# Kernel tuning notes

Measured on AMD Instinct MI355X. Metric: run time of the kernel, lower is better.

## Reference

```python
import jax, jax.numpy as jnp
import numpy as np

P = 16          # patch size
D = 256         # emb dim
NH = 4          # attention heads
DH = D // NH    # head dim
GS = 4          # LE-fusion group size
EPS = 1e-5
ALPHA = 1.0
DELTA = 1.0
BETA = 1.0


def setup_inputs() -> dict:
    key = jax.random.key(0)
    ks = jax.random.split(key, 12)
    B, C, H, W = 8, 1, 256, 256
    s = 0.02
    return {
        "x": jax.random.normal(ks[0], (B, C, H, W), jnp.float32),
        # patch embed as matmul over flattened patches (equivalent to Conv2d k=s=P)
        "Wp": jax.random.normal(ks[1], (C * P * P, D), jnp.float32) * s,
        "bp": jnp.zeros((D,), jnp.float32),
        "ln_g": jnp.ones((D,), jnp.float32),
        "ln_b": jnp.zeros((D,), jnp.float32),
        "Wq": jax.random.normal(ks[2], (D, D), jnp.float32) * s,
        "bq": jnp.zeros((D,), jnp.float32),
        "Wk": jax.random.normal(ks[3], (D, D), jnp.float32) * s,
        "bk": jnp.zeros((D,), jnp.float32),
        "Wv": jax.random.normal(ks[4], (D, D), jnp.float32) * s,
        "bv": jnp.zeros((D,), jnp.float32),
        "Wo": jax.random.normal(ks[5], (D, D), jnp.float32) * s,
        "bo": jnp.zeros((D,), jnp.float32),
    }


def _forward(x, Wp, bp, ln_g, ln_b, Wq, bq, Wk, bk, Wv, bv, Wo, bo):
    B, C, H, W = x.shape
    nh, nw = H // P, W // P
    N = nh * nw
    # --- patch embed: (B,C,H,W) -> (B,N,C*P*P) @ Wp ---
    patches = x.reshape(B, C, nh, P, nw, P).transpose(0, 2, 4, 1, 3, 5)
    patches = patches.reshape(B, N, C * P * P)
    z = patches @ Wp + bp  # (B, N, D)
    # --- NF-Norm: LayerNorm then NeuroFocal scaling ---
    mu = z.mean(-1, keepdims=True)
    var = ((z - mu) ** 2).mean(-1, keepdims=True)
    zn = (z - mu) * jax.lax.rsqrt(var + EPS) * ln_g + ln_b
    mu2 = zn.mean(-1, keepdims=True)
    var2 = ((zn - mu2) ** 2).mean(-1, keepdims=True)
    nf = jnp.abs(zn - mu2).sum(-1, keepdims=True) / (jnp.sqrt(var2 + EPS) + EPS)
    z = zn * (1.0 + nf)
    # --- AG-NFA attention ---
    def split(t):  # (B,N,D) -> (B,NH,N,DH)
        return t.reshape(B, N, NH, DH).transpose(0, 2, 1, 3)
    Q = split(z @ Wq + bq)
    K = split(z @ Wk + bk)
    V = split(z @ Wv + bv)
    qk = jnp.einsum("bhnd,bhmd->bhnm", Q, K)
    logits = qk / jnp.sqrt(jnp.float32(DH))
    mu_q = Q.mean(-1, keepdims=True)
    var_q = ((Q - mu_q) ** 2).mean(-1, keepdims=True)
    sigma_q = jnp.sqrt(var_q + EPS)
    nf_q = jnp.abs(Q - mu_q).sum(-1, keepdims=True) / (sigma_q + EPS)  # (B,NH,N,1)
    # ||Q_n - K_m||^2 = |Q|^2 + |K|^2 - 2 Q.K  (avoids O(N^2*d) diff tensor)
    q2 = (Q * Q).sum(-1)  # (B,NH,N)
    k2 = (K * K).sum(-1)  # (B,NH,N)
    omega = q2[..., :, None] + k2[..., None, :] - 2.0 * qk
    omega = omega / (jnp.exp(-DELTA * nf_q) + 1.0)
    A = jax.nn.softmax(logits - ALPHA * omega, axis=-1)
    out = jnp.einsum("bhnm,bhmd->bhnd", A, V)
    out = out.transpose(0, 2, 1, 3).reshape(B, N, D)
    Y = out @ Wo + bo
    # --- LE-Fusion ---
    G = N // GS
    Yg = Y.reshape(B, G, GS, D)
    E = jnp.linalg.norm(Yg, axis=-1)  # (B,G,GS)
    lam = jax.nn.softmax(BETA * E, axis=-1)[..., None]
    return (lam * Yg).sum(axis=2)  # (B, G, D)


def reference(x, Wp, bp, ln_g, ln_b, Wq, bq, Wk, bk, Wv, bv, Wo, bo):
    return _forward(x, Wp, bp, ln_g, ln_b, Wq, bq, Wk, bk, Wv, bv, Wo, bo)
```

## Files before the change

### kernel.cpp

```cpp
#include <hip/hip_runtime.h>

#define EPSF 1e-5f
#define KSTR 68
#define PSTR 260

#define FMA4(ACC, ZS, WV) \
    ACC.x = fmaf(ZS, WV.x, ACC.x); ACC.y = fmaf(ZS, WV.y, ACC.y); \
    ACC.z = fmaf(ZS, WV.z, ACC.z); ACC.w = fmaf(ZS, WV.w, ACC.w);

__global__ __launch_bounds__(512, 2) void ka_patch_nf_qkv(
    const float* __restrict__ x,
    const float* __restrict__ Wp, const float* __restrict__ bp,
    const float* __restrict__ ln_g, const float* __restrict__ ln_b,
    const float* __restrict__ Wq, const float* __restrict__ bq,
    const float* __restrict__ Wk, const float* __restrict__ bk,
    const float* __restrict__ Wv, const float* __restrict__ bv,
    float* __restrict__ Qg, float* __restrict__ Kg, float* __restrict__ Vg)
{
    extern __shared__ float sm[];
    float* zr = sm;
    float* ps = sm + 2048;

    const int tid = threadIdx.x;
    const int kq = tid >> 7, tg = (tid >> 6) & 1, ln = tid & 63;
    const int wave = tid >> 6, lane = tid & 63;
    const int tok0 = blockIdx.x * 8;
    const int tg4 = 4 * tg;

    #pragma unroll
    for (int i = 0; i < 4; ++i) {
        int e = tid + 512 * i;
        int t = e >> 8, dd = e & 255;
        int tk = tok0 + t, b = tk >> 8, n = tk & 255;
        int ph = n >> 4, pw = n & 15, p = dd >> 4, q = dd & 15;
        zr[t * 256 + dd] = x[b * 65536 + (ph * 16 + p) * 256 + pw * 16 + q];
    }
    __syncthreads();

    {
        const float* wr = Wp + kq * 16384 + 4 * ln;
        const float* zb = zr + tg4 * 256 + kq * 64;
        float4 a0 = make_float4(0.f,0.f,0.f,0.f), a1 = a0, a2 = a0, a3 = a0;
        #pragma unroll
        for (int kk = 0; kk < 64; kk += 8) {
            float4 w0 = *(const float4*)(wr + (kk + 0) * 256);
            float4 w1 = *(const float4*)(wr + (kk + 1) * 256);
            float4 w2 = *(const float4*)(wr + (kk + 2) * 256);
            float4 w3 = *(const float4*)(wr + (kk + 3) * 256);
            float4 w4 = *(const float4*)(wr + (kk + 4) * 256);
            float4 w5 = *(const float4*)(wr + (kk + 5) * 256);
            float4 w6 = *(const float4*)(wr + (kk + 6) * 256);
            float4 w7 = *(const float4*)(wr + (kk + 7) * 256);
            float4 zA0 = *(const float4*)(zb + 0 * 256 + kk);
            float4 zA1 = *(const float4*)(zb + 0 * 256 + kk + 4);
            float4 zB0 = *(const float4*)(zb + 1 * 256 + kk);
            float4 zB1 = *(const float4*)(zb + 1 * 256 + kk + 4);
            float4 zC0 = *(const float4*)(zb + 2 * 256 + kk);
            float4 zC1 = *(const float4*)(zb + 2 * 256 + kk + 4);
            float4 zD0 = *(const float4*)(zb + 3 * 256 + kk);
            float4 zD1 = *(const float4*)(zb + 3 * 256 + kk + 4);
            FMA4(a0, zA0.x, w0) FMA4(a0, zA0.y, w1) FMA4(a0, zA0.z, w2) FMA4(a0, zA0.w, w3)
            FMA4(a0, zA1.x, w4) FMA4(a0, zA1.y, w5) FMA4(a0, zA1.z, w6) FMA4(a0, zA1.w, w7)
            FMA4(a1, zB0.x, w0) FMA4(a1, zB0.y, w1) FMA4(a1, zB0.z, w2) FMA4(a1, zB0.w, w3)
            FMA4(a1, zB1.x, w4) FMA4(a1, zB1.y, w5) FMA4(a1, zB1.z, w6) FMA4(a1, zB1.w, w7)
            FMA4(a2, zC0.x, w0) FMA4(a2, zC0.y, w1) FMA4(a2, zC0.z, w2) FMA4(a2, zC0.w, w3)
            FMA4(a2, zC1.x, w4) FMA4(a2, zC1.y, w5) FMA4(a2, zC1.z, w6) FMA4(a2, zC1.w, w7)
            FMA4(a3, zD0.x, w0) FMA4(a3, zD0.y, w1) FMA4(a3, zD0.z, w2) FMA4(a3, zD0.w, w3)
            FMA4(a3, zD1.x, w4) FMA4(a3, zD1.y, w5) FMA4(a3, zD1.z, w6) FMA4(a3, zD1.w, w7)
        }
        float* pp = ps + kq * 2048 + tg4 * 256 + 4 * ln;
        *(float4*)(pp + 0 * 256) = a0;
        *(float4*)(pp + 1 * 256) = a1;
        *(float4*)(pp + 2 * 256) = a2;
        *(float4*)(pp + 3 * 256) = a3;
    }
    __syncthreads();
    {
        int e = tid * 4;
        float4 u0 = *(float4*)(ps + e);
        float4 u1 = *(float4*)(ps + 2048 + e);
        float4 u2 = *(float4*)(ps + 4096 + e);
        float4 u3 = *(float4*)(ps + 6144 + e);
        float4 bb = *(const float4*)(bp + (e & 255));
        float4 z;
        z.x = (u0.x + u1.x) + (u2.x + u3.x) + bb.x;
        z.y = (u0.y + u1.y) + (u2.y + u3.y) + bb.y;
        z.z = (u0.z + u1.z) + (u2.z + u3.z) + bb.z;
        z.w = (u0.w + u1.w) + (u2.w + u3.w) + bb.w;
        *(float4*)(zr + e) = z;
    }
    __syncthreads();

    {
        float g[4], bb2[4], v[4];
        #pragma unroll
        for (int c = 0; c < 4; ++c) { g[c] = ln_g[lane + 64 * c]; bb2[c] = ln_b[lane + 64 * c]; }
        float s = 0.f, ss = 0.f;
        #pragma unroll
        for (int c = 0; c < 4; ++c) { v[c] = zr[wave * 256 + lane + 64 * c]; s += v[c]; ss += v[c] * v[c]; }
        #pragma unroll
        for (int o = 32; o; o >>= 1) { s += __shfl_xor(s, o); ss += __shfl_xor(ss, o); }
        float mu  = s * (1.f / 256.f);
        float var = ss * (1.f / 256.f) - mu * mu;
        float rs  = rsqrtf(var + EPSF);
        float zn[4]; float s2 = 0.f, ss2 = 0.f;
        #pragma unroll
        for (int c = 0; c < 4; ++c) {
            zn[c] = (v[c] - mu) * rs * g[c] + bb2[c];
            s2 += zn[c]; ss2 += zn[c] * zn[c];
        }
        #pragma unroll
        for (int o = 32; o; o >>= 1) { s2 += __shfl_xor(s2, o); ss2 += __shfl_xor(ss2, o); }
        float mu2  = s2 * (1.f / 256.f);
        float var2 = ss2 * (1.f / 256.f) - mu2 * mu2;
        float as = 0.f;
        #pragma unroll
        for (int c = 0; c < 4; ++c) as += fabsf(zn[c] - mu2);
        #pragma unroll
        for (int o = 32; o; o >>= 1) as += __shfl_xor(as, o);
        float nf = as / (sqrtf(var2 + EPSF) + EPSF);
        float sc = 1.f + nf;
        #pragma unroll
        for (int c = 0; c < 4; ++c) zr[wave * 256 + lane + 64 * c] = zn[c] * sc;
    }
    __syncthreads();

    {
        const float* qr = Wq + kq * 16384 + 4 * ln;
        const float* kr = Wk + kq * 16384 + 4 * ln;
        const float* vr = Wv + kq * 16384 + 4 * ln;
        const float* zb = zr + tg4 * 256 + kq * 64;
        float4 aq0 = make_float4(0.f,0.f,0.f,0.f), aq1 = aq0, aq2 = aq0, aq3 = aq0;
        float4 ak0 = aq0, ak1 = aq0, ak2 = aq0, ak3 = aq0;
        float4 av0 = aq0, av1 = aq0, av2 = aq0, av3 = aq0;
        #pragma unroll
        for (int kk = 0; kk < 64; kk += 4) {
            float4 qw0 = *(const float4*)(qr + (kk + 0) * 256);
            float4 qw1 = *(const float4*)(qr + (kk + 1) * 256);
            float4 qw2 = *(const float4*)(qr + (kk + 2) * 256);
            float4 qw3 = *(const float4*)(qr + (kk + 3) * 256);
            float4 kw0 = *(const float4*)(kr + (kk + 0) * 256);
            float4 kw1 = *(const float4*)(kr + (kk + 1) * 256);
            float4 kw2 = *(const float4*)(kr + (kk + 2) * 256);
            float4 kw3 = *(const float4*)(kr + (kk + 3) * 256);
            float4 vw0 = *(const float4*)(vr + (kk + 0) * 256);
            float4 vw1 = *(const float4*)(vr + (kk + 1) * 256);
            float4 vw2 = *(const float4*)(vr + (kk + 2) * 256);
            float4 vw3 = *(const float4*)(vr + (kk + 3) * 256);
            float4 zA = *(const float4*)(zb + 0 * 256 + kk);
            float4 zB = *(const float4*)(zb + 1 * 256 + kk);
            float4 zC = *(const float4*)(zb + 2 * 256 + kk);
            float4 zD = *(const float4*)(zb + 3 * 256 + kk);
            FMA4(aq0, zA.x, qw0) FMA4(aq0, zA.y, qw1) FMA4(aq0, zA.z, qw2) FMA4(aq0, zA.w, qw3)
            FMA4(ak0, zA.x, kw0) FMA4(ak0, zA.y, kw1) FMA4(ak0, zA.z, kw2) FMA4(ak0, zA.w, kw3)
            FMA4(av0, zA.x, vw0) FMA4(av0, zA.y, vw1) FMA4(av0, zA.z, vw2) FMA4(av0, zA.w, vw3)
            FMA4(aq1, zB.x, qw0) FMA4(aq1, zB.y, qw1) FMA4(aq1, zB.z, qw2) FMA4(aq1, zB.w, qw3)
            FMA4(ak1, zB.x, kw0) FMA4(ak1, zB.y, kw1) FMA4(ak1, zB.z, kw2) FMA4(ak1, zB.w, kw3)
            FMA4(av1, zB.x, vw0) FMA4(av1, zB.y, vw1) FMA4(av1, zB.z, vw2) FMA4(av1, zB.w, vw3)
            FMA4(aq2, zC.x, qw0) FMA4(aq2, zC.y, qw1) FMA4(aq2, zC.z, qw2) FMA4(aq2, zC.w, qw3)
            FMA4(ak2, zC.x, kw0) FMA4(ak2, zC.y, kw1) FMA4(ak2, zC.z, kw2) FMA4(ak2, zC.w, kw3)
            FMA4(av2, zC.x, vw0) FMA4(av2, zC.y, vw1) FMA4(av2, zC.z, vw2) FMA4(av2, zC.w, vw3)
            FMA4(aq3, zD.x, qw0) FMA4(aq3, zD.y, qw1) FMA4(aq3, zD.z, qw2) FMA4(aq3, zD.w, qw3)
            FMA4(ak3, zD.x, kw0) FMA4(ak3, zD.y, kw1) FMA4(ak3, zD.z, kw2) FMA4(ak3, zD.w, kw3)
            FMA4(av3, zD.x, vw0) FMA4(av3, zD.y, vw1) FMA4(av3, zD.z, vw2) FMA4(av3, zD.w, vw3)
        }
        float* pq = ps + kq * 2048 + tg4 * 256 + 4 * ln;
        *(float4*)(pq + 0 * 256) = aq0;
        *(float4*)(pq + 1 * 256) = aq1;
        *(float4*)(pq + 2 * 256) = aq2;
        *(float4*)(pq + 3 * 256) = aq3;
        float* pk = pq + 8192;
        *(float4*)(pk + 0 * 256) = ak0;
        *(float4*)(pk + 1 * 256) = ak1;
        *(float4*)(pk + 2 * 256) = ak2;
        *(float4*)(pk + 3 * 256) = ak3;
        float* pv = pq + 16384;
        *(float4*)(pv + 0 * 256) = av0;
        *(float4*)(pv + 1 * 256) = av1;
        *(float4*)(pv + 2 * 256) = av2;
        *(float4*)(pv + 3 * 256) = av3;
    }
    __syncthreads();

    {
        int e = tid * 4, t = e >> 8, d0 = e & 255;
        int tk = tok0 + t, b = tk >> 8, n = tk & 255;
        int h = d0 >> 6, dh = d0 & 63;
        #pragma unroll
        for (int mat = 0; mat < 3; ++mat) {
            const float* pr = ps + mat * 8192;
            float4 u0 = *(float4*)(pr + e);
            float4 u1 = *(float4*)(pr + 2048 + e);
            float4 u2 = *(float4*)(pr + 4096 + e);
            float4 u3 = *(float4*)(pr + 6144 + e);
            const float* bsrc = (mat == 0) ? bq : (mat == 1) ? bk : bv;
            float4 bb = *(const float4*)(bsrc + d0);
            float4 o;
            o.x = (u0.x + u1.x) + (u2.x + u3.x) + bb.x;
            o.y = (u0.y + u1.y) + (u2.y + u3.y) + bb.y;
            o.z = (u0.z + u1.z) + (u2.z + u3.z) + bb.z;
            o.w = (u0.w + u1.w) + (u2.w + u3.w) + bb.w;
            float* gout = ((mat == 0) ? Qg : (mat == 1) ? Kg : Vg)
                        + ((b * 4 + h) * 256 + n) * 64 + dh;
            *(float4*)gout = o;
        }
    }
}

__global__ __launch_bounds__(512, 2) void kb_attn(
    const float* __restrict__ Qg, const float* __restrict__ Kg,
    const float* __restrict__ Vg, float* __restrict__ Og)
{
    extern __shared__ float lds[];
    float* Kl = lds;
    float* k2 = lds + 256 * KSTR;
    float* Pl = lds;

    const int tid = threadIdx.x;
    const int xcd = blockIdx.x & 7, slot = blockIdx.x >> 3;
    const int bh = xcd * 4 + (slot >> 3);
    const int qt = slot & 7;

    const float* Qb = Qg + (bh * 256 + qt * 32) * 64;
    const float* Kb = Kg + bh * 16384;
    const float* Vb = Vg + bh * 16384;

    const int q = tid >> 4;
    const int r = tid & 15;

    {
        const float4* Ks = (const float4*)Kb;
        #pragma unroll
        for (int i = 0; i < 8; ++i) {
            int flat = tid + 512 * i;
            int row = flat >> 4, c4 = flat & 15;
            *(float4*)(Kl + row * KSTR + c4 * 4) = Ks[flat];
        }
    }
    __syncthreads();

    {
        int row = tid >> 1, half = tid & 1;
        const float* kp = Kl + row * KSTR + half * 32;
        float ssq = 0.f;
        #pragma unroll
        for (int c = 0; c < 8; ++c) {
            float4 kv = *(const float4*)(kp + 4 * c);
            ssq += kv.x*kv.x + kv.y*kv.y + kv.z*kv.z + kv.w*kv.w;
        }
        ssq += __shfl_xor(ssq, 1);
        if (half == 0) k2[row] = ssq;
    }

    float4 Qr[16];
    {
        const float4* Qp = (const float4*)(Qb + q * 64);
        #pragma unroll
        for (int c = 0; c < 16; ++c) Qr[c] = Qp[c];
    }
    float fq, gq, iq;
    {
        float s = 0.f, ss = 0.f;
        #pragma unroll
        for (int c = 0; c < 16; ++c) {
            float4 v = Qr[c];
            s  += v.x + v.y + v.z + v.w;
            ss += v.x*v.x + v.y*v.y + v.z*v.z + v.w*v.w;
        }
        float mu = s * (1.f / 64.f);
        float as = 0.f;
        #pragma unroll
        for (int c = 0; c < 16; ++c) {
            float4 v = Qr[c];
            as += fabsf(v.x - mu) + fabsf(v.y - mu)
                + fabsf(v.z - mu) + fabsf(v.w - mu);
        }
        float var = ss * (1.f / 64.f) - mu * mu;
        float sg  = sqrtf(var + EPSF);
        float nf  = as / (sg + EPSF);
        float inv = 1.f / (__expf(-nf) + 1.f);
        fq = 0.125f + 2.f * inv;
        gq = ss * inv;
        iq = inv;
    }
    __syncthreads();

    float s_[16];
    #pragma unroll
    for (int j = 0; j < 16; ++j) {
        int m = r + 16 * j;
        const float* kp = Kl + m * KSTR;
        float acc = 0.f;
        #pragma unroll
        for (int c = 0; c < 16; ++c) {
            float4 kv = *(const float4*)(kp + 4 * c);
            acc += Qr[c].x*kv.x + Qr[c].y*kv.y + Qr[c].z*kv.z + Qr[c].w*kv.w;
        }
        s_[j] = acc * fq - gq - k2[m] * iq;
    }

    float M = s_[0];
    #pragma unroll
    for (int j = 1; j < 16; ++j) M = fmaxf(M, s_[j]);
    #pragma unroll
    for (int o = 1; o < 16; o <<= 1) M = fmaxf(M, __shfl_xor(M, o));
    float L = 0.f;
    #pragma unroll
    for (int j = 0; j < 16; ++j) { s_[j] = __expf(s_[j] - M); L += s_[j]; }
    #pragma unroll
    for (int o = 1; o < 16; o <<= 1) L += __shfl_xor(L, o);
    float invL = 1.f / L;

    __syncthreads();
    #pragma unroll
    for (int j = 0; j < 16; ++j) Pl[q * PSTR + r + 16 * j] = s_[j] * invL;
    __syncthreads();

    float4 a0 = make_float4(0.f, 0.f, 0.f, 0.f);
    const float* pq = Pl + q * PSTR;
    #pragma unroll 8
    for (int m = 0; m < 256; ++m) {
        float pw = pq[m];
        float4 v = *(const float4*)(Vb + m * 64 + 4 * r);
        a0.x = fmaf(pw, v.x, a0.x); a0.y = fmaf(pw, v.y, a0.y);
        a0.z = fmaf(pw, v.z, a0.z); a0.w = fmaf(pw, v.w, a0.w);
    }
    {
        int b = bh >> 2, h = bh & 3;
        int n = qt * 32 + q;
        float* op = Og + (b * 256 + n) * 256 + h * 64 + 4 * r;
        *(float4*)op = a0;
    }
}

__global__ __launch_bounds__(512, 2) void kc_wo_le(
    const float* __restrict__ Og, const float* __restrict__ Wo,
    const float* __restrict__ bo, float* __restrict__ out)
{
    __shared__ __align__(16) float sm[2048 + 8192 + 8];
    float* yr  = sm;
    float* ps  = sm + 2048;
    float* red = sm + 10240;

    const int tid = threadIdx.x;
    const int kq = tid >> 7, tg = (tid >> 6) & 1, ln = tid & 63;
    const int wave = tid >> 6, lane = tid & 63;
    const int tok0 = blockIdx.x * 8;
    const int tg4 = 4 * tg;

    *(float4*)(yr + tid * 4) = *(const float4*)(Og + tok0 * 256 + tid * 4);
    __syncthreads();

    {
        const float* wr = Wo + kq * 16384 + 4 * ln;
        const float* zb = yr + tg4 * 256 + kq * 64;
        float4 a0 = make_float4(0.f,0.f,0.f,0.f), a1 = a0, a2 = a0, a3 = a0;
        #pragma unroll
        for (int kk = 0; kk < 64; kk += 8) {
            float4 w0 = *(const float4*)(wr + (kk + 0) * 256);
            float4 w1 = *(const float4*)(wr + (kk + 1) * 256);
            float4 w2 = *(const float4*)(wr + (kk + 2) * 256);
            float4 w3 = *(const float4*)(wr + (kk + 3) * 256);
            float4 w4 = *(const float4*)(wr + (kk + 4) * 256);
            float4 w5 = *(const float4*)(wr + (kk + 5) * 256);
            float4 w6 = *(const float4*)(wr + (kk + 6) * 256);
            float4 w7 = *(const float4*)(wr + (kk + 7) * 256);
            float4 zA0 = *(const float4*)(zb + 0 * 256 + kk);
            float4 zA1 = *(const float4*)(zb + 0 * 256 + kk + 4);
            float4 zB0 = *(const float4*)(zb + 1 * 256 + kk);
            float4 zB1 = *(const float4*)(zb + 1 * 256 + kk + 4);
            float4 zC0 = *(const float4*)(zb + 2 * 256 + kk);
            float4 zC1 = *(const float4*)(zb + 2 * 256 + kk + 4);
            float4 zD0 = *(const float4*)(zb + 3 * 256 + kk);
            float4 zD1 = *(const float4*)(zb + 3 * 256 + kk + 4);
            FMA4(a0, zA0.x, w0) FMA4(a0, zA0.y, w1) FMA4(a0, zA0.z, w2) FMA4(a0, zA0.w, w3)
            FMA4(a0, zA1.x, w4) FMA4(a0, zA1.y, w5) FMA4(a0, zA1.z, w6) FMA4(a0, zA1.w, w7)
            FMA4(a1, zB0.x, w0) FMA4(a1, zB0.y, w1) FMA4(a1, zB0.z, w2) FMA4(a1, zB0.w, w3)
            FMA4(a1, zB1.x, w4) FMA4(a1, zB1.y, w5) FMA4(a1, zB1.z, w6) FMA4(a1, zB1.w, w7)
            FMA4(a2, zC0.x, w0) FMA4(a2, zC0.y, w1) FMA4(a2, zC0.z, w2) FMA4(a2, zC0.w, w3)
            FMA4(a2, zC1.x, w4) FMA4(a2, zC1.y, w5) FMA4(a2, zC1.z, w6) FMA4(a2, zC1.w, w7)
            FMA4(a3, zD0.x, w0) FMA4(a3, zD0.y, w1) FMA4(a3, zD0.z, w2) FMA4(a3, zD0.w, w3)
            FMA4(a3, zD1.x, w4) FMA4(a3, zD1.y, w5) FMA4(a3, zD1.z, w6) FMA4(a3, zD1.w, w7)
        }
        float* pp = ps + kq * 2048 + tg4 * 256 + 4 * ln;
        *(float4*)(pp + 0 * 256) = a0;
        *(float4*)(pp + 1 * 256) = a1;
        *(float4*)(pp + 2 * 256) = a2;
        *(float4*)(pp + 3 * 256) = a3;
    }
    __syncthreads();
    {
        int e = tid * 4;
        float4 u0 = *(float4*)(ps + e);
        float4 u1 = *(float4*)(ps + 2048 + e);
        float4 u2 = *(float4*)(ps + 4096 + e);
        float4 u3 = *(float4*)(ps + 6144 + e);
        float4 bb = *(const float4*)(bo + (e & 255));
        float4 y;
        y.x = (u0.x + u1.x) + (u2.x + u3.x) + bb.x;
        y.y = (u0.y + u1.y) + (u2.y + u3.y) + bb.y;
        y.z = (u0.z + u1.z) + (u2.z + u3.z) + bb.z;
        y.w = (u0.w + u1.w) + (u2.w + u3.w) + bb.w;
        *(float4*)(yr + e) = y;
    }
    __syncthreads();
    {
        float ssq = 0.f;
        #pragma unroll
        for (int c = 0; c < 4; ++c) {
            float v = yr[wave * 256 + lane + 64 * c];
            ssq += v * v;
        }
        #pragma unroll
        for (int o = 32; o; o >>= 1) ssq += __shfl_xor(ssq, o);
        if (lane == 0) red[wave] = sqrtf(ssq);
    }
    __syncthreads();
    {
        int g = tid >> 8, d = tid & 255;
        float e0 = red[4 * g], e1 = red[4 * g + 1], e2 = red[4 * g + 2], e3 = red[4 * g + 3];
        float m = fmaxf(fmaxf(e0, e1), fmaxf(e2, e3));
        float x0 = __expf(e0 - m), x1 = __expf(e1 - m), x2 = __expf(e2 - m), x3 = __expf(e3 - m);
        float inv = 1.f / (x0 + x1 + x2 + x3);
        float val = (x0 * yr[(4 * g) * 256 + d] + x1 * yr[(4 * g + 1) * 256 + d]
                   + x2 * yr[(4 * g + 2) * 256 + d] + x3 * yr[(4 * g + 3) * 256 + d]) * inv;
        out[(blockIdx.x * 2 + g) * 256 + d] = val;
    }
}

extern "C" void kernel_launch(void* const* d_in, const int* in_sizes, int n_in,
                              void* d_out, int out_size, void* d_ws, size_t ws_size,
                              hipStream_t stream) {
    const float* x    = (const float*)d_in[0];
    const float* Wp   = (const float*)d_in[1];
    const float* bp   = (const float*)d_in[2];
    const float* ln_g = (const float*)d_in[3];
    const float* ln_b = (const float*)d_in[4];
    const float* Wq   = (const float*)d_in[5];
    const float* bq   = (const float*)d_in[6];
    const float* Wk   = (const float*)d_in[7];
    const float* bk   = (const float*)d_in[8];
    const float* Wv   = (const float*)d_in[9];
    const float* bv   = (const float*)d_in[10];
    const float* Wo   = (const float*)d_in[11];
    const float* bo   = (const float*)d_in[12];
    float* out = (float*)d_out;

    float* ws = (float*)d_ws;
    const size_t TKD = 2048 * 64 * 4;
    float* Qg = ws;
    float* Kg = ws + TKD;
    float* Vg = ws + 2 * TKD;
    float* Og = ws + 3 * TKD;

    const int ka_lds = (2048 + 3 * 4 * 2048) * 4;
    const int kb_lds = (256 * KSTR + 256) * 4;
    (void)hipFuncSetAttribute((const void*)ka_patch_nf_qkv,
                              hipFuncAttributeMaxDynamicSharedMemorySize, ka_lds);
    (void)hipFuncSetAttribute((const void*)kb_attn,
                              hipFuncAttributeMaxDynamicSharedMemorySize, kb_lds);

    ka_patch_nf_qkv<<<256, 512, ka_lds, stream>>>(x, Wp, bp, ln_g, ln_b,
                                                  Wq, bq, Wk, bk, Wv, bv, Qg, Kg, Vg);
    kb_attn<<<256, 512, kb_lds, stream>>>(Qg, Kg, Vg, Og);
    kc_wo_le<<<256, 512, 0, stream>>>(Og, Wo, bo, out);
}
```

Baseline: 60.70 us.

## Double block size and split GEMM K-dimension eight ways in projection kernels

The patch-embed/QKV kernel and the Wo/LE-fusion kernel now launch 1024 threads and split each GEMM's reduction dimension across eight thread groups instead of four. Partial sums are combined through LDS by the first 512 threads. The fused QKV pass is replaced by three sequential single-matrix passes, which shrinks LDS and register use. The aim is more parallelism and latency hiding per block, paid for with extra barriers, more partial-sum traffic and some idle threads during the combine and norm phases.

```diff
diff --git a/kernel.cpp b/kernel.cpp
--- a/kernel.cpp
+++ b/kernel.cpp
@@ -8,7 +8,59 @@
     ACC.x = fmaf(ZS, WV.x, ACC.x); ACC.y = fmaf(ZS, WV.y, ACC.y); \
     ACC.z = fmaf(ZS, WV.z, ACC.z); ACC.w = fmaf(ZS, WV.w, ACC.w);
 
-__global__ __launch_bounds__(512, 2) void ka_patch_nf_qkv(
+__device__ __forceinline__ void gemm_pass8(
+    const float* __restrict__ W, const float* __restrict__ zr,
+    float* __restrict__ ps, int kq, int tg4, int ln)
+{
+    const float* wr = W + kq * 8192 + 4 * ln;
+    const float* zb = zr + tg4 * 256 + kq * 32;
+    float4 a0 = make_float4(0.f,0.f,0.f,0.f), a1 = a0, a2 = a0, a3 = a0;
+    #pragma unroll
+    for (int kk = 0; kk < 32; kk += 8) {
+        float4 w0 = *(const float4*)(wr + (kk + 0) * 256);
+        float4 w1 = *(const float4*)(wr + (kk + 1) * 256);
+        float4 w2 = *(const float4*)(wr + (kk + 2) * 256);
+        float4 w3 = *(const float4*)(wr + (kk + 3) * 256);
+        float4 w4 = *(const float4*)(wr + (kk + 4) * 256);
+        float4 w5 = *(const float4*)(wr + (kk + 5) * 256);
+        float4 w6 = *(const float4*)(wr + (kk + 6) * 256);
+        float4 w7 = *(const float4*)(wr + (kk + 7) * 256);
+        float4 zA0 = *(const float4*)(zb + 0 * 256 + kk);
+        float4 zA1 = *(const float4*)(zb + 0 * 256 + kk + 4);
+        float4 zB0 = *(const float4*)(zb + 1 * 256 + kk);
+        float4 zB1 = *(const float4*)(zb + 1 * 256 + kk + 4);
+        float4 zC0 = *(const float4*)(zb + 2 * 256 + kk);
+        float4 zC1 = *(const float4*)(zb + 2 * 256 + kk + 4);
+        float4 zD0 = *(const float4*)(zb + 3 * 256 + kk);
+        float4 zD1 = *(const float4*)(zb + 3 * 256 + kk + 4);
+        FMA4(a0, zA0.x, w0) FMA4(a0, zA0.y, w1) FMA4(a0, zA0.z, w2) FMA4(a0, zA0.w, w3)
+        FMA4(a0, zA1.x, w4) FMA4(a0, zA1.y, w5) FMA4(a0, zA1.z, w6) FMA4(a0, zA1.w, w7)
+        FMA4(a1, zB0.x, w0) FMA4(a1, zB0.y, w1) FMA4(a1, zB0.z, w2) FMA4(a1, zB0.w, w3)
+        FMA4(a1, zB1.x, w4) FMA4(a1, zB1.y, w5) FMA4(a1, zB1.z, w6) FMA4(a1, zB1.w, w7)
+        FMA4(a2, zC0.x, w0) FMA4(a2, zC0.y, w1) FMA4(a2, zC0.z, w2) FMA4(a2, zC0.w, w3)
+        FMA4(a2, zC1.x, w4) FMA4(a2, zC1.y, w5) FMA4(a2, zC1.z, w6) FMA4(a2, zC1.w, w7)
+        FMA4(a3, zD0.x, w0) FMA4(a3, zD0.y, w1) FMA4(a3, zD0.z, w2) FMA4(a3, zD0.w, w3)
+        FMA4(a3, zD1.x, w4) FMA4(a3, zD1.y, w5) FMA4(a3, zD1.z, w6) FMA4(a3, zD1.w, w7)
+    }
+    float* pp = ps + kq * 2048 + tg4 * 256 + 4 * ln;
+    *(float4*)(pp + 0 * 256) = a0;
+    *(float4*)(pp + 1 * 256) = a1;
+    *(float4*)(pp + 2 * 256) = a2;
+    *(float4*)(pp + 3 * 256) = a3;
+}
+
+__device__ __forceinline__ float4 combine8(const float* __restrict__ ps, int e)
+{
+    float4 a = *(const float4*)(ps + e);
+    #pragma unroll
+    for (int kq = 1; kq < 8; ++kq) {
+        float4 u = *(const float4*)(ps + kq * 2048 + e);
+        a.x += u.x; a.y += u.y; a.z += u.z; a.w += u.w;
+    }
+    return a;
+}
+
+__global__ __launch_bounds__(1024, 4) void ka_patch_nf_qkv(
     const float* __restrict__ x,
     const float* __restrict__ Wp, const float* __restrict__ bp,
     const float* __restrict__ ln_g, const float* __restrict__ ln_b,
@@ -27,71 +79,28 @@
     const int tok0 = blockIdx.x * 8;
     const int tg4 = 4 * tg;
 
-    #pragma unroll
-    for (int i = 0; i < 4; ++i) {
-        int e = tid + 512 * i;
+    {
+        int e = tid * 2;
         int t = e >> 8, dd = e & 255;
         int tk = tok0 + t, b = tk >> 8, n = tk & 255;
         int ph = n >> 4, pw = n & 15, p = dd >> 4, q = dd & 15;
-        zr[t * 256 + dd] = x[b * 65536 + (ph * 16 + p) * 256 + pw * 16 + q];
-    }
-    __syncthreads();
-
-    {
-        const float* wr = Wp + kq * 16384 + 4 * ln;
-        const float* zb = zr + tg4 * 256 + kq * 64;
-        float4 a0 = make_float4(0.f,0.f,0.f,0.f), a1 = a0, a2 = a0, a3 = a0;
-        #pragma unroll
-        for (int kk = 0; kk < 64; kk += 8) {
-            float4 w0 = *(const float4*)(wr + (kk + 0) * 256);
-            float4 w1 = *(const float4*)(wr + (kk + 1) * 256);
-            float4 w2 = *(const float4*)(wr + (kk + 2) * 256);
-            float4 w3 = *(const float4*)(wr + (kk + 3) * 256);
-            float4 w4 = *(const float4*)(wr + (kk + 4) * 256);
-            float4 w5 = *(const float4*)(wr + (kk + 5) * 256);
-            float4 w6 = *(const float4*)(wr + (kk + 6) * 256);
-            float4 w7 = *(const float4*)(wr + (kk + 7) * 256);
-            float4 zA0 = *(const float4*)(zb + 0 * 256 + kk);
-            float4 zA1 = *(const float4*)(zb + 0 * 256 + kk + 4);
-            float4 zB0 = *(const float4*)(zb + 1 * 256 + kk);
-            float4 zB1 = *(const float4*)(zb + 1 * 256 + kk + 4);
-            float4 zC0 = *(const float4*)(zb + 2 * 256 + kk);
-            float4 zC1 = *(const float4*)(zb + 2 * 256 + kk + 4);
-            float4 zD0 = *(const float4*)(zb + 3 * 256 + kk);
-            float4 zD1 = *(const float4*)(zb + 3 * 256 + kk + 4);
-            FMA4(a0, zA0.x, w0) FMA4(a0, zA0.y, w1) FMA4(a0, zA0.z, w2) FMA4(a0, zA0.w, w3)
-            FMA4(a0, zA1.x, w4) FMA4(a0, zA1.y, w5) FMA4(a0, zA1.z, w6) FMA4(a0, zA1.w, w7)
-            FMA4(a1, zB0.x, w0) FMA4(a1, zB0.y, w1) FMA4(a1, zB0.z, w2) FMA4(a1, zB0.w, w3)
-            FMA4(a1, zB1.x, w4) FMA4(a1, zB1.y, w5) FMA4(a1, zB1.z, w6) FMA4(a1, zB1.w, w7)
-            FMA4(a2, zC0.x, w0) FMA4(a2, zC0.y, w1) FMA4(a2, zC0.z, w2) FMA4(a2, zC0.w, w3)
-            FMA4(a2, zC1.x, w4) FMA4(a2, zC1.y, w5) FMA4(a2, zC1.z, w6) FMA4(a2, zC1.w, w7)
-            FMA4(a3, zD0.x, w0) FMA4(a3, zD0.y, w1) FMA4(a3, zD0.z, w2) FMA4(a3, zD0.w, w3)
-            FMA4(a3, zD1.x, w4) FMA4(a3, zD1.y, w5) FMA4(a3, zD1.z, w6) FMA4(a3, zD1.w, w7)
-        }
-        float* pp = ps + kq * 2048 + tg4 * 256 + 4 * ln;
-        *(float4*)(pp + 0 * 256) = a0;
-        *(float4*)(pp + 1 * 256) = a1;
-        *(float4*)(pp + 2 * 256) = a2;
-        *(float4*)(pp + 3 * 256) = a3;
-    }
-    __syncthreads();
-    {
+        float2 v = *(const float2*)(x + b * 65536 + (ph * 16 + p) * 256 + pw * 16 + q);
+        *(float2*)(zr + e) = v;
+    }
+    __syncthreads();
+
+    gemm_pass8(Wp, zr, ps, kq, tg4, ln);
+    __syncthreads();
+    if (tid < 512) {
         int e = tid * 4;
-        float4 u0 = *(float4*)(ps + e);
-        float4 u1 = *(float4*)(ps + 2048 + e);
-        float4 u2 = *(float4*)(ps + 4096 + e);
-        float4 u3 = *(float4*)(ps + 6144 + e);
+        float4 a = combine8(ps, e);
         float4 bb = *(const float4*)(bp + (e & 255));
-        float4 z;
-        z.x = (u0.x + u1.x) + (u2.x + u3.x) + bb.x;
-        z.y = (u0.y + u1.y) + (u2.y + u3.y) + bb.y;
-        z.z = (u0.z + u1.z) + (u2.z + u3.z) + bb.z;
-        z.w = (u0.w + u1.w) + (u2.w + u3.w) + bb.w;
-        *(float4*)(zr + e) = z;
-    }
-    __syncthreads();
-
-    {
+        a.x += bb.x; a.y += bb.y; a.z += bb.z; a.w += bb.w;
+        *(float4*)(zr + e) = a;
+    }
+    __syncthreads();
+
+    if (wave < 8) {
         float g[4], bb2[4], v[4];
         #pragma unroll
         for (int c = 0; c < 4; ++c) { g[c] = ln_g[lane + 64 * c]; bb2[c] = ln_b[lane + 64 * c]; }
@@ -126,83 +135,38 @@
     __syncthreads();
 
     {
-        const float* qr = Wq + kq * 16384 + 4 * ln;
-        const float* kr = Wk + kq * 16384 + 4 * ln;
-        const float* vr = Wv + kq * 16384 + 4 * ln;
-        const float* zb = zr + tg4 * 256 + kq * 64;
-        float4 aq0 = make_float4(0.f,0.f,0.f,0.f), aq1 = aq0, aq2 = aq0, aq3 = aq0;
-        float4 ak0 = aq0, ak1 = aq0, ak2 = aq0, ak3 = aq0;
-        float4 av0 = aq0, av1 = aq0, av2 = aq0, av3 = aq0;
-        #pragma unroll
-        for (int kk = 0; kk < 64; kk += 4) {
-            float4 qw0 = *(const float4*)(qr + (kk + 0) * 256);
-            float4 qw1 = *(const float4*)(qr + (kk + 1) * 256);
-            float4 qw2 = *(const float4*)(qr + (kk + 2) * 256);
-            float4 qw3 = *(const float4*)(qr + (kk + 3) * 256);
-            float4 kw0 = *(const float4*)(kr + (kk + 0) * 256);
-            float4 kw1 = *(const float4*)(kr + (kk + 1) * 256);
-            float4 kw2 = *(const float4*)(kr + (kk + 2) * 256);
-            float4 kw3 = *(const float4*)(kr + (kk + 3) * 256);
-            float4 vw0 = *(const float4*)(vr + (kk + 0) * 256);
-            float4 vw1 = *(const float4*)(vr + (kk + 1) * 256);
-            float4 vw2 = *(const float4*)(vr + (kk + 2) * 256);
-            float4 vw3 = *(const float4*)(vr + (kk + 3) * 256);
-            float4 zA = *(const float4*)(zb + 0 * 256 + kk);
-            float4 zB = *(const float4*)(zb + 1 * 256 + kk);
-            float4 zC = *(const float4*)(zb + 2 * 256 + kk);
-            float4 zD = *(const float4*)(zb + 3 * 256 + kk);
-            FMA4(aq0, zA.x, qw0) FMA4(aq0, zA.y, qw1) FMA4(aq0, zA.z, qw2) FMA4(aq0, zA.w, qw3)
-            FMA4(ak0, zA.x, kw0) FMA4(ak0, zA.y, kw1) FMA4(ak0, zA.z, kw2) FMA4(ak0, zA.w, kw3)
-            FMA4(av0, zA.x, vw0) FMA4(av0, zA.y, vw1) FMA4(av0, zA.z, vw2) FMA4(av0, zA.w, vw3)
-            FMA4(aq1, zB.x, qw0) FMA4(aq1, zB.y, qw1) FMA4(aq1, zB.z, qw2) FMA4(aq1, zB.w, qw3)
-            FMA4(ak1, zB.x, kw0) FMA4(ak1, zB.y, kw1) FMA4(ak1, zB.z, kw2) FMA4(ak1, zB.w, kw3)
-            FMA4(av1, zB.x, vw0) FMA4(av1, zB.y, vw1) FMA4(av1, zB.z, vw2) FMA4(av1, zB.w, vw3)
-            FMA4(aq2, zC.x, qw0) FMA4(aq2, zC.y, qw1) FMA4(aq2, zC.z, qw2) FMA4(aq2, zC.w, qw3)
-            FMA4(ak2, zC.x, kw0) FMA4(ak2, zC.y, kw1) FMA4(ak2, zC.z, kw2) FMA4(ak2, zC.w, kw3)
-            FMA4(av2, zC.x, vw0) FMA4(av2, zC.y, vw1) FMA4(av2, zC.z, vw2) FMA4(av2, zC.w, vw3)
-            FMA4(aq3, zD.x, qw0) FMA4(aq3, zD.y, qw1) FMA4(aq3, zD.z, qw2) FMA4(aq3, zD.w, qw3)
-            FMA4(ak3, zD.x, kw0) FMA4(ak3, zD.y, kw1) FMA4(ak3, zD.z, kw2) FMA4(ak3, zD.w, kw3)
-            FMA4(av3, zD.x, vw0) FMA4(av3, zD.y, vw1) FMA4(av3, zD.z, vw2) FMA4(av3, zD.w, vw3)
-        }
-        float* pq = ps + kq * 2048 + tg4 * 256 + 4 * ln;
-        *(float4*)(pq + 0 * 256) = aq0;
-        *(float4*)(pq + 1 * 256) = aq1;
-        *(float4*)(pq + 2 * 256) = aq2;
-        *(float4*)(pq + 3 * 256) = aq3;
-        float* pk = pq + 8192;
-        *(float4*)(pk + 0 * 256) = ak0;
-        *(float4*)(pk + 1 * 256) = ak1;
-        *(float4*)(pk + 2 * 256) = ak2;
-        *(float4*)(pk + 3 * 256) = ak3;
-        float* pv = pq + 16384;
-        *(float4*)(pv + 0 * 256) = av0;
-        *(float4*)(pv + 1 * 256) = av1;
-        *(float4*)(pv + 2 * 256) = av2;
-        *(float4*)(pv + 3 * 256) = av3;
-    }
-    __syncthreads();
-
-    {
         int e = tid * 4, t = e >> 8, d0 = e & 255;
         int tk = tok0 + t, b = tk >> 8, n = tk & 255;
         int h = d0 >> 6, dh = d0 & 63;
-        #pragma unroll
-        for (int mat = 0; mat < 3; ++mat) {
-            const float* pr = ps + mat * 8192;
-            float4 u0 = *(float4*)(pr + e);
-            float4 u1 = *(float4*)(pr + 2048 + e);
-            float4 u2 = *(float4*)(pr + 4096 + e);
-            float4 u3 = *(float4*)(pr + 6144 + e);
-            const float* bsrc = (mat == 0) ? bq : (mat == 1) ? bk : bv;
-            float4 bb = *(const float4*)(bsrc + d0);
-            float4 o;
-            o.x = (u0.x + u1.x) + (u2.x + u3.x) + bb.x;
-            o.y = (u0.y + u1.y) + (u2.y + u3.y) + bb.y;
-            o.z = (u0.z + u1.z) + (u2.z + u3.z) + bb.z;
-            o.w = (u0.w + u1.w) + (u2.w + u3.w) + bb.w;
-            float* gout = ((mat == 0) ? Qg : (mat == 1) ? Kg : Vg)
-                        + ((b * 4 + h) * 256 + n) * 64 + dh;
-            *(float4*)gout = o;
+        const long goff = ((long)(b * 4 + h) * 256 + n) * 64 + dh;
+
+        gemm_pass8(Wq, zr, ps, kq, tg4, ln);
+        __syncthreads();
+        if (tid < 512) {
+            float4 a = combine8(ps, e);
+            float4 bb = *(const float4*)(bq + d0);
+            a.x += bb.x; a.y += bb.y; a.z += bb.z; a.w += bb.w;
+            *(float4*)(Qg + goff) = a;
+        }
+        __syncthreads();
+
+        gemm_pass8(Wk, zr, ps, kq, tg4, ln);
+        __syncthreads();
+        if (tid < 512) {
+            float4 a = combine8(ps, e);
+            float4 bb = *(const float4*)(bk + d0);
+            a.x += bb.x; a.y += bb.y; a.z += bb.z; a.w += bb.w;
+            *(float4*)(Kg + goff) = a;
+        }
+        __syncthreads();
+
+        gemm_pass8(Wv, zr, ps, kq, tg4, ln);
+        __syncthreads();
+        if (tid < 512) {
+            float4 a = combine8(ps, e);
+            float4 bb = *(const float4*)(bv + d0);
+            a.x += bb.x; a.y += bb.y; a.z += bb.z; a.w += bb.w;
+            *(float4*)(Vg + goff) = a;
         }
     }
 }
@@ -333,14 +297,14 @@
     }
 }
 
-__global__ __launch_bounds__(512, 2) void kc_wo_le(
+__global__ __launch_bounds__(1024, 4) void kc_wo_le(
     const float* __restrict__ Og, const float* __restrict__ Wo,
     const float* __restrict__ bo, float* __restrict__ out)
 {
-    __shared__ __align__(16) float sm[2048 + 8192 + 8];
+    extern __shared__ float sm[];
     float* yr  = sm;
     float* ps  = sm + 2048;
-    float* red = sm + 10240;
+    float* red = sm + 18432;
 
     const int tid = threadIdx.x;
     const int kq = tid >> 7, tg = (tid >> 6) & 1, ln = tid & 63;
@@ -348,63 +312,20 @@
     const int tok0 = blockIdx.x * 8;
     const int tg4 = 4 * tg;
 
-    *(float4*)(yr + tid * 4) = *(const float4*)(Og + tok0 * 256 + tid * 4);
-    __syncthreads();
-
-    {
-        const float* wr = Wo + kq * 16384 + 4 * ln;
-        const float* zb = yr + tg4 * 256 + kq * 64;
-        float4 a0 = make_float4(0.f,0.f,0.f,0.f), a1 = a0, a2 = a0, a3 = a0;
-        #pragma unroll
-        for (int kk = 0; kk < 64; kk += 8) {
-            float4 w0 = *(const float4*)(wr + (kk + 0) * 256);
-            float4 w1 = *(const float4*)(wr + (kk + 1) * 256);
-            float4 w2 = *(const float4*)(wr + (kk + 2) * 256);
-            float4 w3 = *(const float4*)(wr + (kk + 3) * 256);
-            float4 w4 = *(const float4*)(wr + (kk + 4) * 256);
-            float4 w5 = *(const float4*)(wr + (kk + 5) * 256);
-            float4 w6 = *(const float4*)(wr + (kk + 6) * 256);
-            float4 w7 = *(const float4*)(wr + (kk + 7) * 256);
-            float4 zA0 = *(const float4*)(zb + 0 * 256 + kk);
-            float4 zA1 = *(const float4*)(zb + 0 * 256 + kk + 4);
-            float4 zB0 = *(const float4*)(zb + 1 * 256 + kk);
-            float4 zB1 = *(const float4*)(zb + 1 * 256 + kk + 4);
-            float4 zC0 = *(const float4*)(zb + 2 * 256 + kk);
-            float4 zC1 = *(const float4*)(zb + 2 * 256 + kk + 4);
-            float4 zD0 = *(const float4*)(zb + 3 * 256 + kk);
-            float4 zD1 = *(const float4*)(zb + 3 * 256 + kk + 4);
-            FMA4(a0, zA0.x, w0) FMA4(a0, zA0.y, w1) FMA4(a0, zA0.z, w2) FMA4(a0, zA0.w, w3)
-            FMA4(a0, zA1.x, w4) FMA4(a0, zA1.y, w5) FMA4(a0, zA1.z, w6) FMA4(a0, zA1.w, w7)
-            FMA4(a1, zB0.x, w0) FMA4(a1, zB0.y, w1) FMA4(a1, zB0.z, w2) FMA4(a1, zB0.w, w3)
-            FMA4(a1, zB1.x, w4) FMA4(a1, zB1.y, w5) FMA4(a1, zB1.z, w6) FMA4(a1, zB1.w, w7)
-            FMA4(a2, zC0.x, w0) FMA4(a2, zC0.y, w1) FMA4(a2, zC0.z, w2) FMA4(a2, zC0.w, w3)
-            FMA4(a2, zC1.x, w4) FMA4(a2, zC1.y, w5) FMA4(a2, zC1.z, w6) FMA4(a2, zC1.w, w7)
-            FMA4(a3, zD0.x, w0) FMA4(a3, zD0.y, w1) FMA4(a3, zD0.z, w2) FMA4(a3, zD0.w, w3)
-            FMA4(a3, zD1.x, w4) FMA4(a3, zD1.y, w5) FMA4(a3, zD1.z, w6) FMA4(a3, zD1.w, w7)
-        }
-        float* pp = ps + kq * 2048 + tg4 * 256 + 4 * ln;
-        *(float4*)(pp + 0 * 256) = a0;
-        *(float4*)(pp + 1 * 256) = a1;
-        *(float4*)(pp + 2 * 256) = a2;
-        *(float4*)(pp + 3 * 256) = a3;
-    }
-    __syncthreads();
-    {
+    *(float2*)(yr + tid * 2) = *(const float2*)(Og + tok0 * 256 + tid * 2);
+    __syncthreads();
+
+    gemm_pass8(Wo, yr, ps, kq, tg4, ln);
+    __syncthreads();
+    if (tid < 512) {
         int e = tid * 4;
-        float4 u0 = *(float4*)(ps + e);
-        float4 u1 = *(float4*)(ps + 2048 + e);
-        float4 u2 = *(float4*)(ps + 4096 + e);
-        float4 u3 = *(float4*)(ps + 6144 + e);
+        float4 a = combine8(ps, e);
         float4 bb = *(const float4*)(bo + (e & 255));
-        float4 y;
-        y.x = (u0.x + u1.x) + (u2.x + u3.x) + bb.x;
-        y.y = (u0.y + u1.y) + (u2.y + u3.y) + bb.y;
-        y.z = (u0.z + u1.z) + (u2.z + u3.z) + bb.z;
-        y.w = (u0.w + u1.w) + (u2.w + u3.w) + bb.w;
-        *(float4*)(yr + e) = y;
-    }
-    __syncthreads();
-    {
+        a.x += bb.x; a.y += bb.y; a.z += bb.z; a.w += bb.w;
+        *(float4*)(yr + e) = a;
+    }
+    __syncthreads();
+    if (wave < 8) {
         float ssq = 0.f;
         #pragma unroll
         for (int c = 0; c < 4; ++c) {
@@ -416,7 +337,7 @@
         if (lane == 0) red[wave] = sqrtf(ssq);
     }
     __syncthreads();
-    {
+    if (tid < 512) {
         int g = tid >> 8, d = tid & 255;
         float e0 = red[4 * g], e1 = red[4 * g + 1], e2 = red[4 * g + 2], e3 = red[4 * g + 3];
         float m = fmaxf(fmaxf(e0, e1), fmaxf(e2, e3));
@@ -453,15 +374,18 @@
     float* Vg = ws + 2 * TKD;
     float* Og = ws + 3 * TKD;
 
-    const int ka_lds = (2048 + 3 * 4 * 2048) * 4;
+    const int ka_lds = (2048 + 16384) * 4;
     const int kb_lds = (256 * KSTR + 256) * 4;
+    const int kc_lds = (2048 + 16384 + 8) * 4;
     (void)hipFuncSetAttribute((const void*)ka_patch_nf_qkv,
                               hipFuncAttributeMaxDynamicSharedMemorySize, ka_lds);
     (void)hipFuncSetAttribute((const void*)kb_attn,
                               hipFuncAttributeMaxDynamicSharedMemorySize, kb_lds);
-
-    ka_patch_nf_qkv<<<256, 512, ka_lds, stream>>>(x, Wp, bp, ln_g, ln_b,
-                                                  Wq, bq, Wk, bk, Wv, bv, Qg, Kg, Vg);
+    (void)hipFuncSetAttribute((const void*)kc_wo_le,
+                              hipFuncAttributeMaxDynamicSharedMemorySize, kc_lds);
+
+    ka_patch_nf_qkv<<<256, 1024, ka_lds, stream>>>(x, Wp, bp, ln_g, ln_b,
+                                                   Wq, bq, Wk, bk, Wv, bv, Qg, Kg, Vg);
     kb_attn<<<256, 512, kb_lds, stream>>>(Qg, Kg, Vg, Og);
-    kc_wo_le<<<256, 512, 0, stream>>>(Og, Wo, bo, out);
-}
+    kc_wo_le<<<256, 1024, kc_lds, stream>>>(Og, Wo, bo, out);
+}
```

Result: slower. 61.95 us (+2.1%).

## Split patch-embed/NF-norm from QKV projection and retile QKV per head

Applied to the files above, without the earlier changes.

The fused patch/NF-norm/QKV kernel is split in two. The first kernel writes the normalized embeddings z to a workspace buffer. The second computes QKV per (batch, head, 32-token tile), so each block reads only a 64-column slice of each weight matrix and reuses it across 32 tokens. The attention PV stage is also rewritten to store P transposed in LDS with a padded stride and to map threads to query/dim-chunk pairs. This adds a kernel launch and a global round trip for z in exchange for better weight reuse and a different LDS access pattern.

```diff
diff --git a/kernel.cpp b/kernel.cpp
--- a/kernel.cpp
+++ b/kernel.cpp
@@ -2,22 +2,18 @@
 
 #define EPSF 1e-5f
 #define KSTR 68
-#define PSTR 260
 
 #define FMA4(ACC, ZS, WV) \
     ACC.x = fmaf(ZS, WV.x, ACC.x); ACC.y = fmaf(ZS, WV.y, ACC.y); \
     ACC.z = fmaf(ZS, WV.z, ACC.z); ACC.w = fmaf(ZS, WV.w, ACC.w);
 
-__global__ __launch_bounds__(512, 2) void ka_patch_nf_qkv(
+__global__ __launch_bounds__(512, 2) void ka1_patch_nf(
     const float* __restrict__ x,
     const float* __restrict__ Wp, const float* __restrict__ bp,
     const float* __restrict__ ln_g, const float* __restrict__ ln_b,
-    const float* __restrict__ Wq, const float* __restrict__ bq,
-    const float* __restrict__ Wk, const float* __restrict__ bk,
-    const float* __restrict__ Wv, const float* __restrict__ bv,
-    float* __restrict__ Qg, float* __restrict__ Kg, float* __restrict__ Vg)
+    float* __restrict__ zg)
 {
-    extern __shared__ float sm[];
+    __shared__ __align__(16) float sm[2048 + 8192];
     float* zr = sm;
     float* ps = sm + 2048;
 
@@ -125,11 +121,44 @@
     }
     __syncthreads();
 
-    {
-        const float* qr = Wq + kq * 16384 + 4 * ln;
-        const float* kr = Wk + kq * 16384 + 4 * ln;
-        const float* vr = Wv + kq * 16384 + 4 * ln;
-        const float* zb = zr + tg4 * 256 + kq * 64;
+    *(float4*)(zg + tok0 * 256 + tid * 4) = *(float4*)(zr + tid * 4);
+}
+
+__global__ __launch_bounds__(512, 2) void ka2_qkv(
+    const float* __restrict__ zg,
+    const float* __restrict__ Wq, const float* __restrict__ bq,
+    const float* __restrict__ Wk, const float* __restrict__ bk,
+    const float* __restrict__ Wv, const float* __restrict__ bv,
+    float* __restrict__ Qg, float* __restrict__ Kg, float* __restrict__ Vg)
+{
+    extern __shared__ float sm[];
+    float* zt = sm;
+    float* ps = sm + 8192;
+
+    const int tid = threadIdx.x;
+    const int bid = blockIdx.x;
+    const int xcd = bid & 7, slot = bid >> 3;
+    const int h = xcd & 3;
+    const int b = (xcd >> 2) * 4 + (slot & 3);
+    const int n0 = (slot >> 2) * 32;
+
+    const float* zsrc = zg + (b * 256 + n0) * 256;
+    #pragma unroll
+    for (int i = 0; i < 4; ++i) {
+        int e = (tid + 512 * i) * 4;
+        *(float4*)(zt + e) = *(const float4*)(zsrc + e);
+    }
+    __syncthreads();
+
+    const int kq = tid >> 7;
+    const int tokg = (tid >> 4) & 7;
+    const int col = tid & 15;
+
+    {
+        const float* qr = Wq + kq * 16384 + h * 64 + 4 * col;
+        const float* kr = Wk + kq * 16384 + h * 64 + 4 * col;
+        const float* vr = Wv + kq * 16384 + h * 64 + 4 * col;
+        const float* zb = zt + tokg * 1024 + kq * 64;
         float4 aq0 = make_float4(0.f,0.f,0.f,0.f), aq1 = aq0, aq2 = aq0, aq3 = aq0;
         float4 ak0 = aq0, ak1 = aq0, ak2 = aq0, ak3 = aq0;
         float4 av0 = aq0, av1 = aq0, av2 = aq0, av3 = aq0;
@@ -164,44 +193,43 @@
             FMA4(ak3, zD.x, kw0) FMA4(ak3, zD.y, kw1) FMA4(ak3, zD.z, kw2) FMA4(ak3, zD.w, kw3)
             FMA4(av3, zD.x, vw0) FMA4(av3, zD.y, vw1) FMA4(av3, zD.z, vw2) FMA4(av3, zD.w, vw3)
         }
-        float* pq = ps + kq * 2048 + tg4 * 256 + 4 * ln;
-        *(float4*)(pq + 0 * 256) = aq0;
-        *(float4*)(pq + 1 * 256) = aq1;
-        *(float4*)(pq + 2 * 256) = aq2;
-        *(float4*)(pq + 3 * 256) = aq3;
+        float* pq = ps + kq * 2048 + tokg * 256 + 4 * col;
+        *(float4*)(pq + 0 * 64) = aq0;
+        *(float4*)(pq + 1 * 64) = aq1;
+        *(float4*)(pq + 2 * 64) = aq2;
+        *(float4*)(pq + 3 * 64) = aq3;
         float* pk = pq + 8192;
-        *(float4*)(pk + 0 * 256) = ak0;
-        *(float4*)(pk + 1 * 256) = ak1;
-        *(float4*)(pk + 2 * 256) = ak2;
-        *(float4*)(pk + 3 * 256) = ak3;
+        *(float4*)(pk + 0 * 64) = ak0;
+        *(float4*)(pk + 1 * 64) = ak1;
+        *(float4*)(pk + 2 * 64) = ak2;
+        *(float4*)(pk + 3 * 64) = ak3;
         float* pv = pq + 16384;
-        *(float4*)(pv + 0 * 256) = av0;
-        *(float4*)(pv + 1 * 256) = av1;
-        *(float4*)(pv + 2 * 256) = av2;
-        *(float4*)(pv + 3 * 256) = av3;
-    }
-    __syncthreads();
-
-    {
-        int e = tid * 4, t = e >> 8, d0 = e & 255;
-        int tk = tok0 + t, b = tk >> 8, n = tk & 255;
-        int h = d0 >> 6, dh = d0 & 63;
+        *(float4*)(pv + 0 * 64) = av0;
+        *(float4*)(pv + 1 * 64) = av1;
+        *(float4*)(pv + 2 * 64) = av2;
+        *(float4*)(pv + 3 * 64) = av3;
+    }
+    __syncthreads();
+
+    {
+        int e = tid * 4;
+        int tok = e >> 6, d = e & 63;
+        long row = (long)(b * 4 + h) * 256 + n0 + tok;
         #pragma unroll
         for (int mat = 0; mat < 3; ++mat) {
             const float* pr = ps + mat * 8192;
-            float4 u0 = *(float4*)(pr + e);
-            float4 u1 = *(float4*)(pr + 2048 + e);
-            float4 u2 = *(float4*)(pr + 4096 + e);
-            float4 u3 = *(float4*)(pr + 6144 + e);
+            float4 u0 = *(const float4*)(pr + e);
+            float4 u1 = *(const float4*)(pr + 2048 + e);
+            float4 u2 = *(const float4*)(pr + 4096 + e);
+            float4 u3 = *(const float4*)(pr + 6144 + e);
             const float* bsrc = (mat == 0) ? bq : (mat == 1) ? bk : bv;
-            float4 bb = *(const float4*)(bsrc + d0);
+            float4 bb = *(const float4*)(bsrc + h * 64 + d);
             float4 o;
             o.x = (u0.x + u1.x) + (u2.x + u3.x) + bb.x;
             o.y = (u0.y + u1.y) + (u2.y + u3.y) + bb.y;
             o.z = (u0.z + u1.z) + (u2.z + u3.z) + bb.z;
             o.w = (u0.w + u1.w) + (u2.w + u3.w) + bb.w;
-            float* gout = ((mat == 0) ? Qg : (mat == 1) ? Kg : Vg)
-                        + ((b * 4 + h) * 256 + n) * 64 + dh;
+            float* gout = ((mat == 0) ? Qg : (mat == 1) ? Kg : Vg) + row * 64 + d;
             *(float4*)gout = o;
         }
     }
@@ -214,7 +242,7 @@
     extern __shared__ float lds[];
     float* Kl = lds;
     float* k2 = lds + 256 * KSTR;
-    float* Pl = lds;
+    float* Pt = lds;
 
     const int tid = threadIdx.x;
     const int xcd = blockIdx.x & 7, slot = blockIdx.x >> 3;
@@ -313,22 +341,26 @@
 
     __syncthreads();
     #pragma unroll
-    for (int j = 0; j < 16; ++j) Pl[q * PSTR + r + 16 * j] = s_[j] * invL;
-    __syncthreads();
-
-    float4 a0 = make_float4(0.f, 0.f, 0.f, 0.f);
-    const float* pq = Pl + q * PSTR;
-    #pragma unroll 8
-    for (int m = 0; m < 256; ++m) {
-        float pw = pq[m];
-        float4 v = *(const float4*)(Vb + m * 64 + 4 * r);
-        a0.x = fmaf(pw, v.x, a0.x); a0.y = fmaf(pw, v.y, a0.y);
-        a0.z = fmaf(pw, v.z, a0.z); a0.w = fmaf(pw, v.w, a0.w);
-    }
-    {
+    for (int j = 0; j < 16; ++j) Pt[(r + 16 * j) * 33 + q] = s_[j] * invL;
+    __syncthreads();
+
+    {
+        const int w  = tid >> 6;
+        const int lq = tid & 31;
+        const int hi = (tid >> 5) & 1;
+        const int d0 = w * 8 + hi * 4;
+        const float* Vp = Vb + d0;
+        float4 a0 = make_float4(0.f, 0.f, 0.f, 0.f);
+        #pragma unroll 8
+        for (int m = 0; m < 256; ++m) {
+            float pw = Pt[m * 33 + lq];
+            float4 v = *(const float4*)(Vp + m * 64);
+            a0.x = fmaf(pw, v.x, a0.x); a0.y = fmaf(pw, v.y, a0.y);
+            a0.z = fmaf(pw, v.z, a0.z); a0.w = fmaf(pw, v.w, a0.w);
+        }
         int b = bh >> 2, h = bh & 3;
-        int n = qt * 32 + q;
-        float* op = Og + (b * 256 + n) * 256 + h * 64 + 4 * r;
+        int n = qt * 32 + lq;
+        float* op = Og + (b * 256 + n) * 256 + h * 64 + d0;
         *(float4*)op = a0;
     }
 }
@@ -447,21 +479,24 @@
     float* out = (float*)d_out;
 
     float* ws = (float*)d_ws;
-    const size_t TKD = 2048 * 64 * 4;
-    float* Qg = ws;
-    float* Kg = ws + TKD;
-    float* Vg = ws + 2 * TKD;
-    float* Og = ws + 3 * TKD;
-
-    const int ka_lds = (2048 + 3 * 4 * 2048) * 4;
-    const int kb_lds = (256 * KSTR + 256) * 4;
-    (void)hipFuncSetAttribute((const void*)ka_patch_nf_qkv,
-                              hipFuncAttributeMaxDynamicSharedMemorySize, ka_lds);
+    const size_t TKD = 2048 * 64;
+    float* zg = ws;
+    float* Qg = ws + 2048 * 256;
+    float* Kg = Qg + TKD * 4;
+    Qg = ws + 524288;
+    Kg = ws + 524288 * 2;
+    float* Vg = ws + 524288 * 3;
+    float* Og = ws + 524288 * 4;
+
+    const int ka2_lds = (8192 + 24576) * 4;
+    const int kb_lds  = (256 * KSTR + 256) * 4;
+    (void)hipFuncSetAttribute((const void*)ka2_qkv,
+                              hipFuncAttributeMaxDynamicSharedMemorySize, ka2_lds);
     (void)hipFuncSetAttribute((const void*)kb_attn,
                               hipFuncAttributeMaxDynamicSharedMemorySize, kb_lds);
 
-    ka_patch_nf_qkv<<<256, 512, ka_lds, stream>>>(x, Wp, bp, ln_g, ln_b,
-                                                  Wq, bq, Wk, bk, Wv, bv, Qg, Kg, Vg);
+    ka1_patch_nf<<<256, 512, 0, stream>>>(x, Wp, bp, ln_g, ln_b, zg);
+    ka2_qkv<<<256, 512, ka2_lds, stream>>>(zg, Wq, bq, Wk, bk, Wv, bv, Qg, Kg, Vg);
     kb_attn<<<256, 512, kb_lds, stream>>>(Qg, Kg, Vg, Og);
     kc_wo_le<<<256, 512, 0, stream>>>(Og, Wo, bo, out);
 }
```

Result: slower. 63.20 us (+4.1%).
